# Performance work log

Hardware: AMD Instinct MI355X
Metric: run time of the kernel (lower is better)

Reference implementation:

```python
import jax, jax.numpy as jnp
import numpy as np

DIM = 1024
HEADS = 16
DIM_HEAD = 64
INNER = HEADS * DIM_HEAD  # 1024
EPS = 1e-5


def setup_inputs() -> dict:
    key = jax.random.key(0)
    ks = jax.random.split(key, 8)
    b, n = 2, 2048
    x = jax.random.normal(ks[0], (b, n, DIM), dtype=jnp.float32)
    s = 0.02
    return {
        "x": x,
        "ln_g": jnp.ones((DIM,), jnp.float32),
        "ln_b": jnp.zeros((DIM,), jnp.float32),
        "Wq": jax.random.normal(ks[1], (DIM, INNER), jnp.float32) * s,
        "Wkv": jax.random.normal(ks[2], (DIM, 2 * INNER), jnp.float32) * s,
        "mix_pre": jax.random.normal(ks[3], (HEADS, HEADS), jnp.float32),
        "mix_post": jax.random.normal(ks[4], (HEADS, HEADS), jnp.float32),
        "Wout": jax.random.normal(ks[5], (INNER, DIM), jnp.float32) * s,
        "bout": jnp.zeros((DIM,), jnp.float32),
    }


def reference(x, ln_g, ln_b, Wq, Wkv, mix_pre, mix_post, Wout, bout):
    b, n, _ = x.shape
    h, d = HEADS, DIM_HEAD
    scale = d ** -0.5
    # LayerNorm
    mu = jnp.mean(x, axis=-1, keepdims=True)
    var = jnp.var(x, axis=-1, keepdims=True)
    xn = (x - mu) * jax.lax.rsqrt(var + EPS) * ln_g + ln_b
    # projections; context = xn (no external context)
    q = (xn @ Wq).reshape(b, n, h, d).transpose(0, 2, 1, 3)
    kv = xn @ Wkv
    k = kv[..., :INNER].reshape(b, n, h, d).transpose(0, 2, 1, 3)
    v = kv[..., INNER:].reshape(b, n, h, d).transpose(0, 2, 1, 3)
    dots = jnp.einsum('bhid,bhjd->bhij', q, k) * scale
    dots = jnp.einsum('bhij,hg->bgij', dots, mix_pre)  # pre-softmax head mixing
    attn = jax.nn.softmax(dots, axis=-1)
    attn = jnp.einsum('bhij,hg->bgij', attn, mix_post)  # post-softmax head mixing
    out = jnp.einsum('bhij,bhjd->bhid', attn, v)
    out = out.transpose(0, 2, 1, 3).reshape(b, n, INNER)
    return out @ Wout + bout
```

## Files before the change

### kernel.cpp

```cpp
#include <hip/hip_runtime.h>


#define NSEQ 2048
#define DIM  1024
#define NH   16
#define DH   64
#define L2E  1.4426950408889634f
#define MH2  11.541560327111708f

typedef unsigned short u16;
typedef unsigned int   u32;
typedef __attribute__((ext_vector_type(4))) float  f32x4;
typedef __attribute__((ext_vector_type(8))) __bf16 bf16x8;
typedef __attribute__((ext_vector_type(4))) u32    u32x4;
typedef __attribute__((ext_vector_type(2))) u32    u32x2;

__device__ __forceinline__ u16 f2bf(float f) {
  u32 u = __builtin_bit_cast(u32, f);
  u += 0x7fffu + ((u >> 16) & 1u);
  return (u16)(u >> 16);
}

__device__ __forceinline__ f32x4 mfma16(u32x4 a, u32x4 b, f32x4 c) {
  return __builtin_amdgcn_mfma_f32_16x16x32_bf16(
      __builtin_bit_cast(bf16x8, a), __builtin_bit_cast(bf16x8, b), c, 0, 0, 0);
}

__launch_bounds__(256)
__global__ void ln_kernel(const float* __restrict__ x, const float* __restrict__ g,
                          const float* __restrict__ bv, u16* __restrict__ xn) {
  const int row = blockIdx.x, t = threadIdx.x;
  const float4 v = ((const float4*)(x + (size_t)row * DIM))[t];
  float s  = v.x + v.y + v.z + v.w;
  float ss = v.x * v.x + v.y * v.y + v.z * v.z + v.w * v.w;
#pragma unroll
  for (int m = 32; m; m >>= 1) { s += __shfl_xor(s, m); ss += __shfl_xor(ss, m); }
  __shared__ float red[8];
  if ((t & 63) == 0) { red[(t >> 6) * 2] = s; red[(t >> 6) * 2 + 1] = ss; }
  __syncthreads();
  s  = red[0] + red[2] + red[4] + red[6];
  ss = red[1] + red[3] + red[5] + red[7];
  const float mu  = s * (1.0f / DIM);
  const float var = ss * (1.0f / DIM) - mu * mu;
  const float rs  = rsqrtf(var + 1e-5f);
  const float4 gg = ((const float4*)g)[t];
  const float4 bb = ((const float4*)bv)[t];
  ushort4 o;
  o.x = f2bf((v.x - mu) * rs * gg.x + bb.x);
  o.y = f2bf((v.y - mu) * rs * gg.y + bb.y);
  o.z = f2bf((v.z - mu) * rs * gg.z + bb.z);
  o.w = f2bf((v.w - mu) * rs * gg.w + bb.w);
  ((ushort4*)(xn + (size_t)row * DIM))[t] = o;
}

__launch_bounds__(256)
__global__ void wcvt_t(const float* __restrict__ W, u16* __restrict__ WT, int K, int N) {
  __shared__ float tile[32][33];
  const int t = threadIdx.x;
  const int k0 = blockIdx.x * 32, n0 = blockIdx.y * 32;
  {
    int ki = t >> 3, nq = t & 7;
    const float4 v = *(const float4*)(W + (size_t)(k0 + ki) * N + n0 + nq * 4);
    tile[ki][nq * 4 + 0] = v.x; tile[ki][nq * 4 + 1] = v.y;
    tile[ki][nq * 4 + 2] = v.z; tile[ki][nq * 4 + 3] = v.w;
  }
  __syncthreads();
  {
    int ni = t >> 3, kq = t & 7;
    ushort4 o;
    o.x = f2bf(tile[kq * 4 + 0][ni]); o.y = f2bf(tile[kq * 4 + 1][ni]);
    o.z = f2bf(tile[kq * 4 + 2][ni]); o.w = f2bf(tile[kq * 4 + 3][ni]);
    *(ushort4*)(WT + (size_t)(n0 + ni) * K + k0 + kq * 4) = o;
  }
}

__launch_bounds__(256)
__global__ void v_transpose(const u16* __restrict__ kv, u16* __restrict__ VT) {
  __shared__ u16 tile[32][72];
  const int t = threadIdx.x;
  const int n0 = blockIdx.x * 32, gh = blockIdx.y, b = blockIdx.z;
  {
    int i = t >> 3, dq = t & 7;
    u32x4 v = *(const u32x4*)(kv + ((size_t)(b * NSEQ + n0 + i)) * (2 * DIM)
                              + DIM + gh * DH + dq * 8);
    *(u32x4*)(&tile[i][dq * 8]) = v;
  }
  __syncthreads();
  {
    int d = t >> 2, nq = t & 3;
    u32x4 ov;
    ov.x = (u32)tile[nq * 8 + 0][d] | ((u32)tile[nq * 8 + 1][d] << 16);
    ov.y = (u32)tile[nq * 8 + 2][d] | ((u32)tile[nq * 8 + 3][d] << 16);
    ov.z = (u32)tile[nq * 8 + 4][d] | ((u32)tile[nq * 8 + 5][d] << 16);
    ov.w = (u32)tile[nq * 8 + 6][d] | ((u32)tile[nq * 8 + 7][d] << 16);
    *(u32x4*)(VT + ((size_t)((b * NH + gh) * DH + d)) * NSEQ + n0 + nq * 8) = ov;
  }
}

template<int OUTF32, int BIAS>
__launch_bounds__(256)
__global__ void gemm_bt(const u16* __restrict__ A, const u16* __restrict__ BT,
                        void* __restrict__ Cp, const float* __restrict__ bias,
                        float alpha, int M, int N, int K) {
  __shared__ u16 As[128 * 32];
  __shared__ u16 Bs[128 * 32];
  const int t = threadIdx.x, lane = t & 63, r = lane & 15, q = lane >> 4;
  const int m0 = blockIdx.x * 128, n0 = blockIdx.y * 128;
  f32x4 acc[4][4] = {};
  u32x4 ra[2], rb[2];

  auto loadAB = [&](int k0) {
#pragma unroll
    for (int c = 0; c < 2; c++) {
      int u = t + 256 * c;
      int row = u >> 2, col = (u & 3) * 8;
      ra[c] = *(const u32x4*)(A  + (size_t)(m0 + row) * K + k0 + col);
      rb[c] = *(const u32x4*)(BT + (size_t)(n0 + row) * K + k0 + col);
    }
  };
  auto storeAB = [&]() {
#pragma unroll
    for (int c = 0; c < 2; c++) {
      int u = t + 256 * c;
      int row = u >> 2, col = (u & 3) * 8;
      *(u32x4*)(As + row * 32 + col) = ra[c];
      *(u32x4*)(Bs + row * 32 + col) = rb[c];
    }
  };

  loadAB(0);
  const int wr = (t >> 7) * 64;
  const int wc = ((t >> 6) & 1) * 64;
  for (int k0 = 0; k0 < K; k0 += 32) {
    storeAB();
    __syncthreads();
    if (k0 + 32 < K) loadAB(k0 + 32);
    u32x4 af[4], bf[4];
#pragma unroll
    for (int mc = 0; mc < 4; mc++)
      af[mc] = *(const u32x4*)(As + (wr + mc * 16 + r) * 32 + q * 8);
#pragma unroll
    for (int nc = 0; nc < 4; nc++)
      bf[nc] = *(const u32x4*)(Bs + (wc + nc * 16 + r) * 32 + q * 8);
#pragma unroll
    for (int mc = 0; mc < 4; mc++)
#pragma unroll
      for (int nc = 0; nc < 4; nc++)
        acc[mc][nc] = mfma16(af[mc], bf[nc], acc[mc][nc]);
    __syncthreads();
  }
#pragma unroll
  for (int mc = 0; mc < 4; mc++) {
#pragma unroll
    for (int nc = 0; nc < 4; nc++) {
#pragma unroll
      for (int e = 0; e < 4; e++) {
        int row = m0 + wr + mc * 16 + q * 4 + e;
        int col = n0 + wc + nc * 16 + r;
        float v = acc[mc][nc][e] * alpha;
        if (BIAS) v += bias[col];
        if (OUTF32) ((float*)Cp)[(size_t)row * N + col] = v;
        else        ((u16*)Cp)[(size_t)row * N + col]   = f2bf(v);
      }
    }
  }
}

template<int PASSB>
__launch_bounds__(512, 4)
__global__ void attn_v3(const u16* __restrict__ qb, const u16* __restrict__ kvb,
                        const u16* __restrict__ vtb,
                        const float* __restrict__ mixpre, const float* __restrict__ mixpost,
                        float* __restrict__ l_part, float* __restrict__ U_part) {
  __shared__ u16 Sb[32 * 264];
  __shared__ u16 P3b[PASSB ? 16 * 648 : 16];
  const int t = threadIdx.x, w = t >> 6, lane = t & 63, r = lane & 15, qd = lane >> 4;
  const int bid = blockIdx.x;
  const int jh = bid & 1, b = (bid >> 1) & 1;
  const int i0 = (bid >> 2) << 4;
  const f32x4 zero4 = {0.0f, 0.0f, 0.0f, 0.0f};

  u32x4 qf[2][2];
#pragma unroll
  for (int hh = 0; hh < 2; hh++)
#pragma unroll
    for (int kc = 0; kc < 2; kc++)
      qf[hh][kc] = *(const u32x4*)(qb + ((size_t)(b * NSEQ + i0 + r)) * DIM
                                   + (2 * w + hh) * DH + kc * 32 + qd * 8);

  auto build_mix = [&](const float* m) {
    u32x4 f;
    u16 c[8];
#pragma unroll
    for (int e = 0; e < 8; e++)
      c[e] = f2bf(0.5f * m[(8 * (qd & 1) + e) * NH + r]);
    f.x = (u32)c[0] | ((u32)c[1] << 16);
    f.y = (u32)c[2] | ((u32)c[3] << 16);
    f.z = (u32)c[4] | ((u32)c[5] << 16);
    f.w = (u32)c[6] | ((u32)c[7] << 16);
    return f;
  };
  const u32x4 mpf = build_mix(mixpre);
  u32x4 mpostf = {0, 0, 0, 0};
  float rl[2] = {0.0f, 0.0f};
  if (PASSB) {
    mpostf = build_mix(mixpost);
#pragma unroll
    for (int ii = 0; ii < 2; ii++) {
      int ig = i0 + 2 * w + ii;
      float lv = l_part[((size_t)(b * NH + r)) * NSEQ + ig]
               + l_part[((size_t)((2 + b) * NH + r)) * NSEQ + ig];
      rl[ii] = 1.0f / lv;
    }
  }

  f32x4 U[2][4];
#pragma unroll
  for (int hh = 0; hh < 2; hh++)
#pragma unroll
    for (int dc = 0; dc < 4; dc++) U[hh][dc] = zero4;
  float lsum0 = 0.0f, lsum1 = 0.0f;

  for (int s = 0; s < 32; s++) {
    const int j0 = jh * 1024 + s * 32;
    const int gran = (w >> 2) ^ ((r >> 2) & 1) ^ (qd & 1);
#pragma unroll
    for (int jc = 0; jc < 2; jc++) {
      f32x4 sh[2];
#pragma unroll
      for (int hh = 0; hh < 2; hh++) {
        const u16* kr = kvb + ((size_t)(b * NSEQ + j0 + jc * 16 + r)) * (2 * DIM)
                        + (2 * w + hh) * DH + qd * 8;
        u32x4 kf0 = *(const u32x4*)(kr);
        u32x4 kf1 = *(const u32x4*)(kr + 32);
        sh[hh] = mfma16(qf[hh][0], kf0, zero4);
        sh[hh] = mfma16(qf[hh][1], kf1, sh[hh]);
      }
#pragma unroll
      for (int e = 0; e < 4; e++) {
        u32 pk = (u32)f2bf(sh[0][e]) | ((u32)f2bf(sh[1][e]) << 16);
        *(u32*)(Sb + (2 * (4 * qd + e) + jc) * 264 + r * 16 + gran * 8 + 2 * (w & 3)) = pk;
      }
    }
    __syncthreads();

#pragma unroll
    for (int cc = 0; cc < 4; cc++) {
      const int ch = 4 * w + cc, ii = cc >> 1, jc = cc & 1;
      const int gs = (qd & 1) ^ ((r >> 2) & 1) ^ ((ch >> 3) & 1);
      u32x4 af = *(const u32x4*)(Sb + ch * 264 + r * 16 + gs * 8);
      f32x4 d2 = mfma16(af, mpf, zero4);
      float p0 = exp2f(fmaf(d2[0], L2E, -MH2));
      float p1 = exp2f(fmaf(d2[1], L2E, -MH2));
      float p2 = exp2f(fmaf(d2[2], L2E, -MH2));
      float p3 = exp2f(fmaf(d2[3], L2E, -MH2));
      if (!PASSB) {
        if (ii == 0) lsum0 += (p0 + p1) + (p2 + p3);
        else         lsum1 += (p0 + p1) + (p2 + p3);
      } else {
        const float sc = rl[ii];
        const int granw = (r >> 3) ^ (qd & 1) ^ ((ch >> 3) & 1);
        Sb[ch * 264 + (4 * qd + 0) * 16 + granw * 8 + (r & 7)] = f2bf(p0 * sc);
        Sb[ch * 264 + (4 * qd + 1) * 16 + granw * 8 + (r & 7)] = f2bf(p1 * sc);
        Sb[ch * 264 + (4 * qd + 2) * 16 + granw * 8 + (r & 7)] = f2bf(p2 * sc);
        Sb[ch * 264 + (4 * qd + 3) * 16 + granw * 8 + (r & 7)] = f2bf(p3 * sc);
        u32x4 ef = *(const u32x4*)(Sb + ch * 264 + r * 16 + gs * 8);
        f32x4 d3 = mfma16(ef, mpostf, zero4);
        const int i = 2 * w + ii;
        u32x2 pk;
        pk.x = (u32)f2bf(d3[0]) | ((u32)f2bf(d3[1]) << 16);
        pk.y = (u32)f2bf(d3[2]) | ((u32)f2bf(d3[3]) << 16);
        *(u32x2*)(P3b + r * 648 + i * 40 + jc * 16 + 4 * qd) = pk;
      }
    }
    __syncthreads();

    if (PASSB) {
#pragma unroll
      for (int hh = 0; hh < 2; hh++) {
        const int g = 2 * w + hh;
        u32x4 paf = *(const u32x4*)(P3b + g * 648 + r * 40 + 8 * qd);
#pragma unroll
        for (int dc = 0; dc < 4; dc++) {
          u32x4 vf = *(const u32x4*)(vtb
              + ((size_t)((b * NH + g) * DH + dc * 16 + r)) * NSEQ + j0 + 8 * qd);
          U[hh][dc] = mfma16(paf, vf, U[hh][dc]);
        }
      }
    }
  }

  if (!PASSB) {
    lsum0 += __shfl_xor(lsum0, 16); lsum0 += __shfl_xor(lsum0, 32);
    lsum1 += __shfl_xor(lsum1, 16); lsum1 += __shfl_xor(lsum1, 32);
    if (qd == 0) {
      l_part[((size_t)((jh * 2 + b) * NH + r)) * NSEQ + i0 + 2 * w]     = lsum0;
      l_part[((size_t)((jh * 2 + b) * NH + r)) * NSEQ + i0 + 2 * w + 1] = lsum1;
    }
  } else {
#pragma unroll
    for (int hh = 0; hh < 2; hh++)
#pragma unroll
      for (int dc = 0; dc < 4; dc++)
#pragma unroll
        for (int e = 0; e < 4; e++)
          U_part[((size_t)((jh * 2 + b) * NSEQ + i0 + 4 * qd + e)) * DIM
                 + (2 * w + hh) * DH + dc * 16 + r] = U[hh][dc][e];
  }
}

__launch_bounds__(256)
__global__ void combine(const float* __restrict__ U, u16* __restrict__ oat) {
  const size_t x = ((size_t)blockIdx.x * 256 + threadIdx.x) * 4;
  float4 a = *(const float4*)(U + x);
  float4 c = *(const float4*)(U + x + (size_t)4 * 1024 * 1024);
  u32x2 pk;
  pk.x = (u32)f2bf(a.x + c.x) | ((u32)f2bf(a.y + c.y) << 16);
  pk.y = (u32)f2bf(a.z + c.z) | ((u32)f2bf(a.w + c.w) << 16);
  *(u32x2*)(oat + x) = pk;
}

extern "C" void kernel_launch(void* const* d_in, const int* in_sizes, int n_in,
                              void* d_out, int out_size, void* d_ws, size_t ws_size,
                              hipStream_t stream) {
  (void)in_sizes; (void)n_in; (void)out_size; (void)ws_size;
  const float* x       = (const float*)d_in[0];
  const float* ln_g    = (const float*)d_in[1];
  const float* ln_b    = (const float*)d_in[2];
  const float* Wq      = (const float*)d_in[3];
  const float* Wkv     = (const float*)d_in[4];
  const float* mixpre  = (const float*)d_in[5];
  const float* mixpost = (const float*)d_in[6];
  const float* Wout    = (const float*)d_in[7];
  const float* bout    = (const float*)d_in[8];
  float* out = (float*)d_out;

  char* p = (char*)d_ws;
  auto alloc = [&](size_t bytes) {
    char* rp = p; p += (bytes + 255) & ~(size_t)255; return rp;
  };
  u16*   xn    = (u16*)alloc((size_t)4096 * 1024 * 2);
  u16*   WqT   = (u16*)alloc((size_t)1024 * 1024 * 2);
  u16*   WkvT  = (u16*)alloc((size_t)2048 * 1024 * 2);
  u16*   WoutT = (u16*)alloc((size_t)1024 * 1024 * 2);
  u16*   qb    = (u16*)alloc((size_t)4096 * 1024 * 2);
  u16*   kvb   = (u16*)alloc((size_t)4096 * 2048 * 2);
  u16*   VTb   = (u16*)alloc((size_t)2 * NH * DH * NSEQ * 2);
  float* lpart = (float*)alloc((size_t)4 * NH * NSEQ * 4);
  float* Upart = (float*)alloc((size_t)4 * NSEQ * DIM * 4);
  u16*   oat   = (u16*)alloc((size_t)4096 * 1024 * 2);

  ln_kernel<<<4096, 256, 0, stream>>>(x, ln_g, ln_b, xn);
  wcvt_t<<<dim3(32, 32), 256, 0, stream>>>(Wq,   WqT,   1024, 1024);
  wcvt_t<<<dim3(32, 64), 256, 0, stream>>>(Wkv,  WkvT,  1024, 2048);
  wcvt_t<<<dim3(32, 32), 256, 0, stream>>>(Wout, WoutT, 1024, 1024);
  gemm_bt<0, 0><<<dim3(32, 8),  256, 0, stream>>>(xn, WqT,  qb,  nullptr, 0.125f, 4096, 1024, 1024);
  gemm_bt<0, 0><<<dim3(32, 16), 256, 0, stream>>>(xn, WkvT, kvb, nullptr, 1.0f,   4096, 2048, 1024);
  v_transpose<<<dim3(64, 16, 2), 256, 0, stream>>>(kvb, VTb);
  attn_v3<0><<<512, 512, 0, stream>>>(qb, kvb, VTb, mixpre, mixpost, lpart, Upart);
  attn_v3<1><<<512, 512, 0, stream>>>(qb, kvb, VTb, mixpre, mixpost, lpart, Upart);
  combine<<<4096, 256, 0, stream>>>(Upart, oat);
  gemm_bt<1, 1><<<dim3(32, 8), 256, 0, stream>>>(oat, WoutT, out, bout, 1.0f, 4096, 1024, 1024);
}
```

Before: 547.1 us.

## Split attention passes into specialized kernels with K prefetch and register mixing

Replaces the templated two-pass attention kernel with two specialized kernels. The row-sum pass now handles 32 query rows per block over a quarter of the keys, reusing each K load across twice the queries, and keeps per-head sums in MFMA-layout accumulators. Both kernels prefetch the next K tile into registers across the barrier. The second pass applies post-softmax mixing directly from registers via a swapped-operand MFMA, dropping the LDS write/read round trip. This costs more registers and a larger l_part buffer, and relies on subtle fragment-layout correctness.

```diff
diff --git a/kernel.cpp b/kernel.cpp
--- a/kernel.cpp
+++ b/kernel.cpp
@@ -166,17 +166,124 @@
   }
 }
 
-template<int PASSB>
 __launch_bounds__(512, 4)
-__global__ void attn_v3(const u16* __restrict__ qb, const u16* __restrict__ kvb,
-                        const u16* __restrict__ vtb,
-                        const float* __restrict__ mixpre, const float* __restrict__ mixpost,
-                        float* __restrict__ l_part, float* __restrict__ U_part) {
-  __shared__ u16 Sb[32 * 264];
-  __shared__ u16 P3b[PASSB ? 16 * 648 : 16];
+__global__ void attn_a(const u16* __restrict__ qb, const u16* __restrict__ kvb,
+                       const float* __restrict__ mixpre, float* __restrict__ l_part) {
+  __shared__ u16 Sb[64 * 264];
   const int t = threadIdx.x, w = t >> 6, lane = t & 63, r = lane & 15, qd = lane >> 4;
   const int bid = blockIdx.x;
-  const int jh = bid & 1, b = (bid >> 1) & 1;
+  const int slab = bid & 7, jq = slab >> 1, b = slab & 1;
+  const int i0 = (bid >> 3) << 5;
+  const f32x4 zero4 = {0.0f, 0.0f, 0.0f, 0.0f};
+
+  u32x4 qf[2][2][2];
+#pragma unroll
+  for (int ig = 0; ig < 2; ig++)
+#pragma unroll
+    for (int hh = 0; hh < 2; hh++)
+#pragma unroll
+      for (int kc = 0; kc < 2; kc++)
+        qf[ig][hh][kc] = *(const u32x4*)(qb
+            + ((size_t)(b * NSEQ + i0 + ig * 16 + r)) * DIM
+            + (2 * w + hh) * DH + kc * 32 + qd * 8);
+
+  u32x4 mpf;
+  {
+    u16 c[8];
+#pragma unroll
+    for (int e = 0; e < 8; e++)
+      c[e] = f2bf(0.5f * mixpre[(8 * (qd & 1) + e) * NH + r]);
+    mpf.x = (u32)c[0] | ((u32)c[1] << 16);
+    mpf.y = (u32)c[2] | ((u32)c[3] << 16);
+    mpf.z = (u32)c[4] | ((u32)c[5] << 16);
+    mpf.w = (u32)c[6] | ((u32)c[7] << 16);
+  }
+
+  u32x4 kf[2][2][2];
+  auto loadK = [&](int j0) {
+#pragma unroll
+    for (int hh = 0; hh < 2; hh++)
+#pragma unroll
+      for (int jc = 0; jc < 2; jc++)
+#pragma unroll
+        for (int kc = 0; kc < 2; kc++)
+          kf[hh][jc][kc] = *(const u32x4*)(kvb
+              + ((size_t)(b * NSEQ + j0 + jc * 16 + r)) * (2 * DIM)
+              + (2 * w + hh) * DH + kc * 32 + qd * 8);
+  };
+  loadK(jq * 512);
+
+  f32x4 lacc[4] = {zero4, zero4, zero4, zero4};
+
+  for (int s = 0; s < 16; s++) {
+    const int j0 = jq * 512 + s * 32;
+    const int gran = (w >> 2) ^ ((r >> 2) & 1) ^ (qd & 1);
+#pragma unroll
+    for (int ig = 0; ig < 2; ig++) {
+#pragma unroll
+      for (int jc = 0; jc < 2; jc++) {
+        f32x4 s0 = mfma16(qf[ig][0][0], kf[0][jc][0], zero4);
+        s0 = mfma16(qf[ig][0][1], kf[0][jc][1], s0);
+        f32x4 s1 = mfma16(qf[ig][1][0], kf[1][jc][0], zero4);
+        s1 = mfma16(qf[ig][1][1], kf[1][jc][1], s1);
+#pragma unroll
+        for (int c = 0; c < 4; c++) {
+          const int ch = 2 * (ig * 16 + 4 * qd + c) + jc;
+          u32 pk = (u32)f2bf(s0[c]) | ((u32)f2bf(s1[c]) << 16);
+          *(u32*)(Sb + ch * 264 + r * 16 + gran * 8 + 2 * (w & 3)) = pk;
+        }
+      }
+    }
+    __syncthreads();
+
+    if (s + 1 < 16) loadK(j0 + 32);
+
+#pragma unroll
+    for (int cc = 0; cc < 8; cc++) {
+      const int ch = 8 * w + cc, slot = cc >> 1;
+      const int gs = (qd & 1) ^ ((r >> 2) & 1) ^ ((ch >> 3) & 1);
+      u32x4 af = *(const u32x4*)(Sb + ch * 264 + r * 16 + gs * 8);
+      f32x4 d2 = mfma16(mpf, af, zero4);
+      f32x4 ev;
+      ev[0] = exp2f(fmaf(d2[0], L2E, -MH2));
+      ev[1] = exp2f(fmaf(d2[1], L2E, -MH2));
+      ev[2] = exp2f(fmaf(d2[2], L2E, -MH2));
+      ev[3] = exp2f(fmaf(d2[3], L2E, -MH2));
+      lacc[slot] += ev;
+    }
+    __syncthreads();
+  }
+
+#pragma unroll
+  for (int slot = 0; slot < 4; slot++) {
+#pragma unroll
+    for (int m = 1; m <= 8; m <<= 1) {
+      lacc[slot][0] += __shfl_xor(lacc[slot][0], m);
+      lacc[slot][1] += __shfl_xor(lacc[slot][1], m);
+      lacc[slot][2] += __shfl_xor(lacc[slot][2], m);
+      lacc[slot][3] += __shfl_xor(lacc[slot][3], m);
+    }
+  }
+  if (r == 0) {
+#pragma unroll
+    for (int slot = 0; slot < 4; slot++)
+#pragma unroll
+      for (int c = 0; c < 4; c++)
+        l_part[((size_t)(slab * NH + 4 * qd + c)) * NSEQ + i0 + 4 * w + slot]
+            = lacc[slot][c];
+  }
+}
+
+__launch_bounds__(512, 4)
+__global__ void attn_b(const u16* __restrict__ qb, const u16* __restrict__ kvb,
+                       const u16* __restrict__ vtb,
+                       const float* __restrict__ mixpre, const float* __restrict__ mixpost,
+                       const float* __restrict__ l_part, float* __restrict__ U_part) {
+  __shared__ u16 Sb[32 * 264];
+  __shared__ u16 P3b[16 * 648];
+  const int t = threadIdx.x, w = t >> 6, lane = t & 63, r = lane & 15, qd = lane >> 4;
+  const int bid = blockIdx.x;
+  const int slab4 = bid & 3, jh = slab4 >> 1, b = slab4 & 1;
   const int i0 = (bid >> 2) << 4;
   const f32x4 zero4 = {0.0f, 0.0f, 0.0f, 0.0f};
 
@@ -188,125 +295,120 @@
       qf[hh][kc] = *(const u32x4*)(qb + ((size_t)(b * NSEQ + i0 + r)) * DIM
                                    + (2 * w + hh) * DH + kc * 32 + qd * 8);
 
-  auto build_mix = [&](const float* m) {
-    u32x4 f;
+  u32x4 mpf, mp2f;
+  {
     u16 c[8];
 #pragma unroll
     for (int e = 0; e < 8; e++)
-      c[e] = f2bf(0.5f * m[(8 * (qd & 1) + e) * NH + r]);
-    f.x = (u32)c[0] | ((u32)c[1] << 16);
-    f.y = (u32)c[2] | ((u32)c[3] << 16);
-    f.z = (u32)c[4] | ((u32)c[5] << 16);
-    f.w = (u32)c[6] | ((u32)c[7] << 16);
-    return f;
+      c[e] = f2bf(0.5f * mixpre[(8 * (qd & 1) + e) * NH + r]);
+    mpf.x = (u32)c[0] | ((u32)c[1] << 16);
+    mpf.y = (u32)c[2] | ((u32)c[3] << 16);
+    mpf.z = (u32)c[4] | ((u32)c[5] << 16);
+    mpf.w = (u32)c[6] | ((u32)c[7] << 16);
+#pragma unroll
+    for (int e = 0; e < 8; e++)
+      c[e] = f2bf(0.5f * mixpost[(4 * qd + (e & 3)) * NH + r]);
+    mp2f.x = (u32)c[0] | ((u32)c[1] << 16);
+    mp2f.y = (u32)c[2] | ((u32)c[3] << 16);
+    mp2f.z = (u32)c[4] | ((u32)c[5] << 16);
+    mp2f.w = (u32)c[6] | ((u32)c[7] << 16);
+  }
+
+  float rl[2][4];
+#pragma unroll
+  for (int ii = 0; ii < 2; ii++)
+#pragma unroll
+    for (int c = 0; c < 4; c++) {
+      float lv = 0.0f;
+#pragma unroll
+      for (int jqq = 0; jqq < 4; jqq++)
+        lv += l_part[((size_t)((jqq * 2 + b) * NH + 4 * qd + c)) * NSEQ + i0 + 2 * w + ii];
+      rl[ii][c] = 1.0f / lv;
+    }
+
+  u32x4 kf[2][2][2];
+  auto loadK = [&](int j0) {
+#pragma unroll
+    for (int hh = 0; hh < 2; hh++)
+#pragma unroll
+      for (int jc = 0; jc < 2; jc++)
+#pragma unroll
+        for (int kc = 0; kc < 2; kc++)
+          kf[hh][jc][kc] = *(const u32x4*)(kvb
+              + ((size_t)(b * NSEQ + j0 + jc * 16 + r)) * (2 * DIM)
+              + (2 * w + hh) * DH + kc * 32 + qd * 8);
   };
-  const u32x4 mpf = build_mix(mixpre);
-  u32x4 mpostf = {0, 0, 0, 0};
-  float rl[2] = {0.0f, 0.0f};
-  if (PASSB) {
-    mpostf = build_mix(mixpost);
-#pragma unroll
-    for (int ii = 0; ii < 2; ii++) {
-      int ig = i0 + 2 * w + ii;
-      float lv = l_part[((size_t)(b * NH + r)) * NSEQ + ig]
-               + l_part[((size_t)((2 + b) * NH + r)) * NSEQ + ig];
-      rl[ii] = 1.0f / lv;
-    }
-  }
+  loadK(jh * 1024);
 
   f32x4 U[2][4];
 #pragma unroll
   for (int hh = 0; hh < 2; hh++)
 #pragma unroll
     for (int dc = 0; dc < 4; dc++) U[hh][dc] = zero4;
-  float lsum0 = 0.0f, lsum1 = 0.0f;
 
   for (int s = 0; s < 32; s++) {
     const int j0 = jh * 1024 + s * 32;
     const int gran = (w >> 2) ^ ((r >> 2) & 1) ^ (qd & 1);
 #pragma unroll
     for (int jc = 0; jc < 2; jc++) {
-      f32x4 sh[2];
-#pragma unroll
-      for (int hh = 0; hh < 2; hh++) {
-        const u16* kr = kvb + ((size_t)(b * NSEQ + j0 + jc * 16 + r)) * (2 * DIM)
-                        + (2 * w + hh) * DH + qd * 8;
-        u32x4 kf0 = *(const u32x4*)(kr);
-        u32x4 kf1 = *(const u32x4*)(kr + 32);
-        sh[hh] = mfma16(qf[hh][0], kf0, zero4);
-        sh[hh] = mfma16(qf[hh][1], kf1, sh[hh]);
+      f32x4 s0 = mfma16(qf[0][0], kf[0][jc][0], zero4);
+      s0 = mfma16(qf[0][1], kf[0][jc][1], s0);
+      f32x4 s1 = mfma16(qf[1][0], kf[1][jc][0], zero4);
+      s1 = mfma16(qf[1][1], kf[1][jc][1], s1);
+#pragma unroll
+      for (int c = 0; c < 4; c++) {
+        const int ch = 2 * (4 * qd + c) + jc;
+        u32 pk = (u32)f2bf(s0[c]) | ((u32)f2bf(s1[c]) << 16);
+        *(u32*)(Sb + ch * 264 + r * 16 + gran * 8 + 2 * (w & 3)) = pk;
       }
-#pragma unroll
-      for (int e = 0; e < 4; e++) {
-        u32 pk = (u32)f2bf(sh[0][e]) | ((u32)f2bf(sh[1][e]) << 16);
-        *(u32*)(Sb + (2 * (4 * qd + e) + jc) * 264 + r * 16 + gran * 8 + 2 * (w & 3)) = pk;
-      }
-    }
-    __syncthreads();
+    }
+    __syncthreads();
+
+    if (s + 1 < 32) loadK(j0 + 32);
 
 #pragma unroll
     for (int cc = 0; cc < 4; cc++) {
       const int ch = 4 * w + cc, ii = cc >> 1, jc = cc & 1;
       const int gs = (qd & 1) ^ ((r >> 2) & 1) ^ ((ch >> 3) & 1);
       u32x4 af = *(const u32x4*)(Sb + ch * 264 + r * 16 + gs * 8);
-      f32x4 d2 = mfma16(af, mpf, zero4);
-      float p0 = exp2f(fmaf(d2[0], L2E, -MH2));
-      float p1 = exp2f(fmaf(d2[1], L2E, -MH2));
-      float p2 = exp2f(fmaf(d2[2], L2E, -MH2));
-      float p3 = exp2f(fmaf(d2[3], L2E, -MH2));
-      if (!PASSB) {
-        if (ii == 0) lsum0 += (p0 + p1) + (p2 + p3);
-        else         lsum1 += (p0 + p1) + (p2 + p3);
-      } else {
-        const float sc = rl[ii];
-        const int granw = (r >> 3) ^ (qd & 1) ^ ((ch >> 3) & 1);
-        Sb[ch * 264 + (4 * qd + 0) * 16 + granw * 8 + (r & 7)] = f2bf(p0 * sc);
-        Sb[ch * 264 + (4 * qd + 1) * 16 + granw * 8 + (r & 7)] = f2bf(p1 * sc);
-        Sb[ch * 264 + (4 * qd + 2) * 16 + granw * 8 + (r & 7)] = f2bf(p2 * sc);
-        Sb[ch * 264 + (4 * qd + 3) * 16 + granw * 8 + (r & 7)] = f2bf(p3 * sc);
-        u32x4 ef = *(const u32x4*)(Sb + ch * 264 + r * 16 + gs * 8);
-        f32x4 d3 = mfma16(ef, mpostf, zero4);
-        const int i = 2 * w + ii;
-        u32x2 pk;
-        pk.x = (u32)f2bf(d3[0]) | ((u32)f2bf(d3[1]) << 16);
-        pk.y = (u32)f2bf(d3[2]) | ((u32)f2bf(d3[3]) << 16);
-        *(u32x2*)(P3b + r * 648 + i * 40 + jc * 16 + 4 * qd) = pk;
+      f32x4 d2 = mfma16(mpf, af, zero4);
+      float pv0 = exp2f(fmaf(d2[0], L2E, -MH2)) * rl[ii][0];
+      float pv1 = exp2f(fmaf(d2[1], L2E, -MH2)) * rl[ii][1];
+      float pv2 = exp2f(fmaf(d2[2], L2E, -MH2)) * rl[ii][2];
+      float pv3 = exp2f(fmaf(d2[3], L2E, -MH2)) * rl[ii][3];
+      u32x4 pa;
+      pa.x = (u32)f2bf(pv0) | ((u32)f2bf(pv1) << 16);
+      pa.y = (u32)f2bf(pv2) | ((u32)f2bf(pv3) << 16);
+      pa.z = pa.x; pa.w = pa.y;
+      f32x4 d3 = mfma16(pa, mp2f, zero4);
+      u32x2 pk;
+      pk.x = (u32)f2bf(d3[0]) | ((u32)f2bf(d3[1]) << 16);
+      pk.y = (u32)f2bf(d3[2]) | ((u32)f2bf(d3[3]) << 16);
+      *(u32x2*)(P3b + r * 648 + (2 * w + ii) * 40 + jc * 16 + 4 * qd) = pk;
+    }
+    __syncthreads();
+
+#pragma unroll
+    for (int hh = 0; hh < 2; hh++) {
+      const int g = 2 * w + hh;
+      u32x4 paf = *(const u32x4*)(P3b + g * 648 + r * 40 + 8 * qd);
+#pragma unroll
+      for (int dc = 0; dc < 4; dc++) {
+        u32x4 vf = *(const u32x4*)(vtb
+            + ((size_t)((b * NH + g) * DH + dc * 16 + r)) * NSEQ + j0 + 8 * qd);
+        U[hh][dc] = mfma16(paf, vf, U[hh][dc]);
       }
     }
-    __syncthreads();
-
-    if (PASSB) {
-#pragma unroll
-      for (int hh = 0; hh < 2; hh++) {
-        const int g = 2 * w + hh;
-        u32x4 paf = *(const u32x4*)(P3b + g * 648 + r * 40 + 8 * qd);
-#pragma unroll
-        for (int dc = 0; dc < 4; dc++) {
-          u32x4 vf = *(const u32x4*)(vtb
-              + ((size_t)((b * NH + g) * DH + dc * 16 + r)) * NSEQ + j0 + 8 * qd);
-          U[hh][dc] = mfma16(paf, vf, U[hh][dc]);
-        }
-      }
-    }
-  }
-
-  if (!PASSB) {
-    lsum0 += __shfl_xor(lsum0, 16); lsum0 += __shfl_xor(lsum0, 32);
-    lsum1 += __shfl_xor(lsum1, 16); lsum1 += __shfl_xor(lsum1, 32);
-    if (qd == 0) {
-      l_part[((size_t)((jh * 2 + b) * NH + r)) * NSEQ + i0 + 2 * w]     = lsum0;
-      l_part[((size_t)((jh * 2 + b) * NH + r)) * NSEQ + i0 + 2 * w + 1] = lsum1;
-    }
-  } else {
-#pragma unroll
-    for (int hh = 0; hh < 2; hh++)
-#pragma unroll
-      for (int dc = 0; dc < 4; dc++)
-#pragma unroll
-        for (int e = 0; e < 4; e++)
-          U_part[((size_t)((jh * 2 + b) * NSEQ + i0 + 4 * qd + e)) * DIM
-                 + (2 * w + hh) * DH + dc * 16 + r] = U[hh][dc][e];
-  }
+  }
+
+#pragma unroll
+  for (int hh = 0; hh < 2; hh++)
+#pragma unroll
+    for (int dc = 0; dc < 4; dc++)
+#pragma unroll
+      for (int e = 0; e < 4; e++)
+        U_part[((size_t)((jh * 2 + b) * NSEQ + i0 + 4 * qd + e)) * DIM
+               + (2 * w + hh) * DH + dc * 16 + r] = U[hh][dc][e];
 }
 
 __launch_bounds__(256)
@@ -346,7 +448,7 @@
   u16*   qb    = (u16*)alloc((size_t)4096 * 1024 * 2);
   u16*   kvb   = (u16*)alloc((size_t)4096 * 2048 * 2);
   u16*   VTb   = (u16*)alloc((size_t)2 * NH * DH * NSEQ * 2);
-  float* lpart = (float*)alloc((size_t)4 * NH * NSEQ * 4);
+  float* lpart = (float*)alloc((size_t)8 * NH * NSEQ * 4);
   float* Upart = (float*)alloc((size_t)4 * NSEQ * DIM * 4);
   u16*   oat   = (u16*)alloc((size_t)4096 * 1024 * 2);
 
@@ -357,8 +459,8 @@
   gemm_bt<0, 0><<<dim3(32, 8),  256, 0, stream>>>(xn, WqT,  qb,  nullptr, 0.125f, 4096, 1024, 1024);
   gemm_bt<0, 0><<<dim3(32, 16), 256, 0, stream>>>(xn, WkvT, kvb, nullptr, 1.0f,   4096, 2048, 1024);
   v_transpose<<<dim3(64, 16, 2), 256, 0, stream>>>(kvb, VTb);
-  attn_v3<0><<<512, 512, 0, stream>>>(qb, kvb, VTb, mixpre, mixpost, lpart, Upart);
-  attn_v3<1><<<512, 512, 0, stream>>>(qb, kvb, VTb, mixpre, mixpost, lpart, Upart);
+  attn_a<<<512, 512, 0, stream>>>(qb, kvb, mixpre, lpart);
+  attn_b<<<512, 512, 0, stream>>>(qb, kvb, VTb, mixpre, mixpost, lpart, Upart);
   combine<<<4096, 256, 0, stream>>>(Upart, oat);
   gemm_bt<1, 1><<<dim3(32, 8), 256, 0, stream>>>(oat, WoutT, out, bout, 1.0f, 4096, 1024, 1024);
 }
```

Result: faster. 499.5 us (-8.7%).
